# Kernel optimization log

Measured on AMD Instinct MI355X. Metric: run time of the kernel, lower is better.

The kernel has to match this reference:

```python
import jax, jax.numpy as jnp
import numpy as np

N_AGENTS = 16
OBS = 128
STATE = 256
EMBED = 32
NHID = 32
NHEADS = 4
ALPHA = 0.2  # leaky relu slope
NEG = -9.0e15


def gat_layer(h, adj, W, a):
    # h: [B,N,Fin], W: [Fin,Fout], a: [2*Fout,1]  (dropout is identity in eval mode)
    Wh = h @ W                                   # [B,N,Fout]
    f = W.shape[1]
    e = jax.nn.leaky_relu(Wh @ a[:f] + jnp.swapaxes(Wh @ a[f:], 1, 2), ALPHA)  # [B,N,N]
    att = jnp.where(adj > 0, e, NEG)
    att = jax.nn.softmax(att, axis=1)            # faithful to torch dim=1 on [B,N,N]
    return att @ Wh                              # [B,N,Fout]


def gat(x, adj, Wh_heads, a_heads, Wout, aout):
    # Wh_heads: [H,Fin,NHID], a_heads: [H,2*NHID,1]
    heads = jax.vmap(gat_layer, in_axes=(None, None, 0, 0))(x, adj, Wh_heads, a_heads)  # [H,B,N,NHID]
    heads = jax.nn.elu(heads)                    # concat=True layers apply elu
    B, N = x.shape[0], x.shape[1]
    xcat = jnp.transpose(heads, (1, 2, 0, 3)).reshape(B, N, -1)  # [B,N,H*NHID]
    out = gat_layer(xcat, adj, Wout, aout)       # concat=False: no elu inside layer
    out = jax.nn.elu(out)
    return jax.nn.log_softmax(out, axis=1)       # over agent axis, as in torch dim=1


def setup_inputs() -> dict:
    key = jax.random.key(0)
    ks = jax.random.split(key, 20)
    bs, T = 64, 128
    s = 0.05
    inp = {
        "agent_qs": jax.random.normal(ks[0], (bs, T, N_AGENTS), jnp.float32),
        "states": jax.random.normal(ks[1], (bs, T, STATE), jnp.float32),
        "obs_ls": jax.random.normal(ks[2], (bs, T, N_AGENTS, OBS), jnp.float32),
        "adj_ls": jnp.ones((bs, T, N_AGENTS, N_AGENTS), jnp.float32),
        # weight_net: Linear(STATE, N_AGENTS)
        "wn_w": jax.random.normal(ks[3], (N_AGENTS, STATE), jnp.float32) * s,
        "wn_b": jnp.zeros((N_AGENTS,), jnp.float32),
        # hyper_w_1 GAT: 4 heads (OBS->NHID), out (NHID*4 -> N_AGENTS*EMBED)
        "g1_Wh": jax.random.normal(ks[4], (NHEADS, OBS, NHID), jnp.float32) * s,
        "g1_ah": jax.random.normal(ks[5], (NHEADS, 2 * NHID, 1), jnp.float32) * s,
        "g1_Wout": jax.random.normal(ks[6], (NHID * NHEADS, N_AGENTS * EMBED), jnp.float32) * s,
        "g1_aout": jax.random.normal(ks[7], (2 * N_AGENTS * EMBED, 1), jnp.float32) * s,
        # hyper_w_final GAT: 4 heads (OBS->NHID), out (NHID*4 -> EMBED)
        "gf_Wh": jax.random.normal(ks[8], (NHEADS, OBS, NHID), jnp.float32) * s,
        "gf_ah": jax.random.normal(ks[9], (NHEADS, 2 * NHID, 1), jnp.float32) * s,
        "gf_Wout": jax.random.normal(ks[10], (NHID * NHEADS, EMBED), jnp.float32) * s,
        "gf_aout": jax.random.normal(ks[11], (2 * EMBED, 1), jnp.float32) * s,
        # hyper_b_ls: N_AGENTS Linears(STATE -> EMBED), stacked
        "hb_W": jax.random.normal(ks[12], (N_AGENTS, EMBED, STATE), jnp.float32) * s,
        "hb_b": jnp.zeros((N_AGENTS, EMBED), jnp.float32),
        # V: Linear(STATE,EMBED) -> ReLU -> Linear(EMBED,1)
        "v1_w": jax.random.normal(ks[13], (EMBED, STATE), jnp.float32) * s,
        "v1_b": jnp.zeros((EMBED,), jnp.float32),
        "v2_w": jax.random.normal(ks[14], (1, EMBED), jnp.float32) * s,
        "v2_b": jnp.zeros((1,), jnp.float32),
    }
    return inp


def reference(agent_qs, states, obs_ls, adj_ls, wn_w, wn_b,
              g1_Wh, g1_ah, g1_Wout, g1_aout,
              gf_Wh, gf_ah, gf_Wout, gf_aout,
              hb_W, hb_b, v1_w, v1_b, v2_w, v2_b):
    bs = agent_qs.shape[0]
    qs = agent_qs.reshape(-1, N_AGENTS)                 # [B,N]
    st = states.reshape(-1, STATE)                      # [B,S]
    obs = obs_ls.reshape(-1, N_AGENTS, OBS)             # [B,N,OBS]
    adj = adj_ls.reshape(-1, N_AGENTS, N_AGENTS)        # [B,N,N]
    B = qs.shape[0]

    hyper_w1 = jnp.abs(gat(obs, adj, g1_Wh, g1_ah, g1_Wout, g1_aout))   # [B,N,N*E]
    hyper_wf = jnp.abs(gat(obs, adj, gf_Wh, gf_ah, gf_Wout, gf_aout))   # [B,N,E]

    dis = jnp.abs(st @ wn_w.T + wn_b)                   # [B,N]

    w1 = hyper_w1.reshape(B, N_AGENTS, N_AGENTS, EMBED)  # [B,i,n,E]
    b_all = jnp.einsum('bs,nes->bne', st, hb_W) + hb_b   # [B,N,E]
    hidden = jax.nn.elu(jnp.einsum('bn,bine->bie', qs, w1) + b_all)  # [B,N,E]

    v = jax.nn.relu(st @ v1_w.T + v1_b) @ v2_w.T + v2_b  # [B,1]

    y = jnp.einsum('bje,bje->bj', hidden, hyper_wf)       # [B,N]
    q = jnp.einsum('bj,bj->b', y, dis) + v[:, 0]          # [B]
    return q.reshape(bs, -1, 1)
```

## Files before the change

kernel.cpp:

```cpp
#include <hip/hip_runtime.h>
#include <math.h>

#define NAG 16
#define OBSD 128
#define STATED 256
#define ALPHA 0.2f
#define NEGV -9.0e15f
#define BTOT 8192
#define SLOT_H 2432

typedef _Float16 v4h __attribute__((ext_vector_type(4)));
typedef _Float16 v8h __attribute__((ext_vector_type(8)));
typedef float v4f __attribute__((ext_vector_type(4)));

__device__ __forceinline__ float lrelu(float x){ return x > 0.f ? x : ALPHA*x; }
__device__ __forceinline__ float eluf(float x){ return x > 0.f ? x : (__expf(x)-1.f); }

#define MFMA16(A,B,C) __builtin_amdgcn_mfma_f32_16x16x16f16((A),(B),(C),0,0,0)
#define MFMA32(A,B,C) __builtin_amdgcn_mfma_f32_16x16x32_f16((A),(B),(C),0,0,0)

__global__ void prep2_kernel(const float* __restrict__ g1_Wout, const float* __restrict__ g1_aout,
                             const float* __restrict__ gf_Wout, const float* __restrict__ gf_aout,
                             float* __restrict__ wa){
  int k = threadIdx.x;
  float su = 0.f, sv = 0.f;
  for (int c = 0; c < 512; ++c){
    float w = g1_Wout[k*512 + c];
    su += w * g1_aout[c];
    sv += w * g1_aout[512 + c];
  }
  wa[k] = su; wa[128 + k] = sv;
  float fu = 0.f, fv = 0.f;
  for (int c = 0; c < 32; ++c){
    float w = gf_Wout[k*32 + c];
    fu += w * gf_aout[c];
    fv += w * gf_aout[32 + c];
  }
  wa[256 + k] = fu; wa[384 + k] = fv;
}

__global__ void pack_wh_kernel(const float* __restrict__ g1_Wh, const float* __restrict__ gf_Wh,
                               const float* __restrict__ g1_ah, const float* __restrict__ gf_ah,
                               _Float16* __restrict__ dst){
  int idx = blockIdx.x*256 + threadIdx.x;
  if (idx >= 17*2048) return;
  int j = idx & 7, lane = (idx>>3)&63, kk = (idx>>9)&3, nt = idx>>11;
  int k = kk*32 + (lane>>4)*8 + j;
  int li = lane & 15;
  float v;
  if (nt < 16){
    int g = nt>>1, c = (nt&1)*16 + li;
    v = (g<4) ? g1_Wh[(g*OBSD + k)*32 + c] : gf_Wh[((g-4)*OBSD + k)*32 + c];
  } else {
    int g = li>>1, half = li&1;
    const float* W = (g<4)? (g1_Wh + g*OBSD*32) : (gf_Wh + (g-4)*OBSD*32);
    const float* a = ((g<4)? (g1_ah + g*64) : (gf_ah + (g-4)*64)) + half*32;
    float s = 0.f;
    for (int c=0;c<32;++c) s += W[k*32+c]*a[c];
    v = s;
  }
  dst[idx] = (_Float16)v;
}

__global__ void pack_wout_kernel(const float* __restrict__ g1_Wout, const float* __restrict__ gf_Wout,
                                 _Float16* __restrict__ dst1, _Float16* __restrict__ dstf){
  int idx = blockIdx.x*256 + threadIdx.x;
  if (idx < 65536){
    int j = idx&7, lane=(idx>>3)&63, kk=(idx>>9)&3, nt=idx>>11;
    int k = kk*32 + (lane>>4)*8 + j;
    dst1[idx] = (_Float16)g1_Wout[k*512 + nt*16 + (lane&15)];
  } else {
    int i2 = idx - 65536;
    int j=i2&7, lane=(i2>>3)&63, kk=(i2>>9)&3, nt=i2>>11;
    int k = kk*32 + (lane>>4)*8 + j;
    dstf[i2] = (_Float16)gf_Wout[k*32 + nt*16 + (lane&15)];
  }
}

__global__ void pack_wst_kernel(const float* __restrict__ hb_W, const float* __restrict__ wn_w,
                                const float* __restrict__ v1_w, _Float16* __restrict__ dst){
  int idx = blockIdx.x*256 + threadIdx.x;
  if (idx >= 35*4096) return;
  int j = idx&7, lane=(idx>>3)&63, kk=(idx>>9)&7, nt=idx>>12;
  int s = kk*32 + (lane>>4)*8 + j;
  int c = nt*16 + (lane&15);
  float v;
  if (c < 512)      v = hb_W[c*STATED + s];
  else if (c < 528) v = wn_w[(c-512)*STATED + s];
  else              v = v1_w[(c-528)*STATED + s];
  dst[idx] = (_Float16)v;
}

__global__ __launch_bounds__(256) void st_kernel(
    const float* __restrict__ states,
    const _Float16* __restrict__ wstf,
    const float* __restrict__ hb_b, const float* __restrict__ wn_b,
    const float* __restrict__ v1_b, const float* __restrict__ v2_w,
    const float* __restrict__ v2_b,
    float* __restrict__ b_all, float* __restrict__ dis, float* __restrict__ vv){
  __shared__ float vh_s[16*32];
  const int t = threadIdx.x, w = t>>6, lane = t&63, lg = lane>>4, li = lane&15;
  const int b0 = blockIdx.x*16;
  const float* sp = states + (size_t)(b0+li)*STATED + lg*8;
  v8h ast[8];
  #pragma unroll
  for (int kk=0;kk<8;++kk){
    v4f f0 = *reinterpret_cast<const v4f*>(sp + kk*32);
    v4f f1 = *reinterpret_cast<const v4f*>(sp + kk*32 + 4);
    v8h h;
    #pragma unroll
    for (int jj=0;jj<4;++jj){ h[jj]=(_Float16)f0[jj]; h[4+jj]=(_Float16)f1[jj]; }
    ast[kk]=h;
  }
  for (int nt=w; nt<35; nt+=4){
    v4f d = {0.f,0.f,0.f,0.f};
    #pragma unroll
    for (int kk=0;kk<8;++kk){
      v8h bf = *reinterpret_cast<const v8h*>(wstf + (size_t)(((nt*8+kk)<<6)+lane)*8);
      d = MFMA32(ast[kk], bf, d);
    }
    int c = nt*16 + li;
    if (c < 512){
      float bias = hb_b[c];
      #pragma unroll
      for (int r=0;r<4;++r) b_all[(size_t)(b0+lg*4+r)*512 + c] = d[r]+bias;
    } else if (c < 528){
      float bias = wn_b[c-512];
      #pragma unroll
      for (int r=0;r<4;++r) dis[(b0+lg*4+r)*NAG + (c-512)] = fabsf(d[r]+bias);
    } else {
      float bias = v1_b[c-528];
      #pragma unroll
      for (int r=0;r<4;++r) vh_s[(lg*4+r)*32 + (c-528)] = fmaxf(d[r]+bias, 0.f);
    }
  }
  __syncthreads();
  if (t < 16){
    float s = v2_b[0];
    #pragma unroll
    for (int e=0;e<32;++e) s += vh_s[t*32+e]*v2_w[e];
    vv[b0+t] = s;
  }
}

__global__ __launch_bounds__(256,4) void gat_kernel(
    const float* __restrict__ agent_qs,
    const float* __restrict__ obs_ls,
    const float* __restrict__ adj_ls,
    const _Float16* __restrict__ whf,
    const _Float16* __restrict__ wo1f,
    const _Float16* __restrict__ wodf,
    const float* __restrict__ wa_g,
    const float* __restrict__ b_all_ws,
    const float* __restrict__ dis_ws,
    const float* __restrict__ vv_ws,
    float* __restrict__ out){
  __shared__ __align__(16) _Float16 arena_h[4*SLOT_H];
  __shared__ __align__(8)  _Float16 adjh[4*256];
  __shared__ float qs_s[64];

  const int t = threadIdx.x, w = t>>6, lane = t&63, lg = lane>>4, li = lane&15;
  const int bb = blockIdx.x*4;
  const int b = bb + w;
  const int eh = w&1, pb = (w>>1)*2;
  const v4f ZERO4 = {0.f,0.f,0.f,0.f};
  const v4h ONESH = {(_Float16)1.f,(_Float16)1.f,(_Float16)1.f,(_Float16)1.f};

  {
    float4 f = reinterpret_cast<const float4*>(adj_ls + (size_t)bb*256)[t];
    _Float16* ap = adjh + t*4;
    ap[0]=(_Float16)f.x; ap[1]=(_Float16)f.y; ap[2]=(_Float16)f.z; ap[3]=(_Float16)f.w;
  }
  if (t < 64) qs_s[t] = agent_qs[bb*NAG + t];

  _Float16* slot   = arena_h + w*SLOT_H;
  _Float16* att_h  = slot;
  _Float16* uv_h   = slot + 2176;
  _Float16* u2v2_h = slot;
  _Float16* att2_h = slot + 64;
  const _Float16* adjw = adjh + w*256;

  const float* ob = obs_ls + (size_t)b*(NAG*OBSD) + li*OBSD + lg*8;
  v8h aob[4];
  #pragma unroll
  for (int kk=0;kk<4;++kk){
    v4f f0 = *reinterpret_cast<const v4f*>(ob + kk*32);
    v4f f1 = *reinterpret_cast<const v4f*>(ob + kk*32 + 4);
    v8h h;
    #pragma unroll
    for (int jj=0;jj<4;++jj){ h[jj]=(_Float16)f0[jj]; h[4+jj]=(_Float16)f1[jj]; }
    aob[kk]=h;
  }
  v4h whB[16];
  #pragma unroll
  for (int nt=0;nt<16;++nt){
    v4f d = ZERO4;
    #pragma unroll
    for (int kk=0;kk<4;++kk){
      v8h bf = *reinterpret_cast<const v8h*>(whf + (size_t)(((nt*4+kk)<<6) + lane)*8);
      d = MFMA32(aob[kk], bf, d);
    }
    v4h hh;
    #pragma unroll
    for (int r=0;r<4;++r) hh[r]=(_Float16)d[r];
    whB[nt]=hh;
  }
  {
    v4f d = ZERO4;
    #pragma unroll
    for (int kk=0;kk<4;++kk){
      v8h bf = *reinterpret_cast<const v8h*>(whf + (size_t)(((64+kk)<<6) + lane)*8);
      d = MFMA32(aob[kk], bf, d);
    }
    #pragma unroll
    for (int r=0;r<4;++r)
      uv_h[(li>>1)*32 + (li&1)*16 + lg*4 + r] = (_Float16)d[r];
  }

  {
    int cc = lane*2;
    int g = cc>>4, j0 = cc&15;
    float vj0 = (float)uv_h[g*32+16+j0], vj1 = (float)uv_h[g*32+16+j0+1];
    float e0[16], e1[16];
    float s0=0.f, s1=0.f;
    #pragma unroll
    for (int i=0;i<16;++i){
      float u = (float)uv_h[g*32+i];
      union { unsigned u32; _Float16 h[2]; } aa;
      aa.u32 = *reinterpret_cast<const unsigned*>(adjw + i*16 + j0);
      float x0 = lrelu(u+vj0), x1 = lrelu(u+vj1);
      x0 = ((float)aa.h[0] > 0.f) ? x0 : NEGV;
      x1 = ((float)aa.h[1] > 0.f) ? x1 : NEGV;
      x0 = __expf(x0); x1 = __expf(x1);
      e0[i]=x0; e1[i]=x1; s0+=x0; s1+=x1;
    }
    float inv0=1.f/s0, inv1=1.f/s1;
    #pragma unroll
    for (int i=0;i<16;++i){
      union { unsigned u32; _Float16 h[2]; } pk;
      pk.h[0]=(_Float16)(e0[i]*inv0);
      pk.h[1]=(_Float16)(e1[i]*inv1);
      int blk = (j0>>2) ^ ((i>>2)&3);
      *reinterpret_cast<unsigned*>(&att_h[g*272 + i*16 + (blk<<2) + (j0&3)]) = pk.u32;
    }
  }

  v4h xcB[16];
  float p2[4][4];
  #pragma unroll
  for (int k4=0;k4<4;++k4)
    #pragma unroll
    for (int r=0;r<4;++r) p2[k4][r]=0.f;
  {
    const int ablk = (lg ^ ((li>>2)&3)) << 2;
    #pragma unroll
    for (int g=0;g<8;++g){
      v4h afr = *reinterpret_cast<const v4h*>(&att_h[g*272 + li*16 + ablk]);
      int side = g>>2;
      #pragma unroll
      for (int h2=0;h2<2;++h2){
        int nt = g*2+h2;
        v4f d = ZERO4;
        d = MFMA16(afr, whB[nt], d);
        int cl = (nt - side*8)*16 + li;
        float wu = wa_g[side*256 + cl];
        float wv = wa_g[side*256 + 128 + cl];
        v4h hh;
        #pragma unroll
        for (int r=0;r<4;++r){
          float e = eluf(d[r]);
          hh[r]=(_Float16)e;
          p2[side*2][r]   += e*wu;
          p2[side*2+1][r] += e*wv;
        }
        xcB[nt]=hh;
      }
    }
  }
  #pragma unroll
  for (int off=1; off<16; off<<=1)
    #pragma unroll
    for (int k4=0;k4<4;++k4)
      #pragma unroll
      for (int r=0;r<4;++r) p2[k4][r] += __shfl_xor(p2[k4][r], off, 64);
  if (li==0){
    #pragma unroll
    for (int k4=0;k4<4;++k4)
      #pragma unroll
      for (int r=0;r<4;++r) u2v2_h[k4*16 + lg*4 + r] = (_Float16)p2[k4][r];
  }

  if (lane < 32){
    int side = lane>>4, j = lane&15;
    float vj = (float)u2v2_h[side*32 + 16 + j];
    float ev[16]; float ss=0.f;
    #pragma unroll
    for (int i=0;i<16;++i){
      float x = lrelu((float)u2v2_h[side*32 + i] + vj);
      x = ((float)adjw[i*16+j] > 0.f) ? x : NEGV;
      x = __expf(x);
      ev[i]=x; ss+=x;
    }
    float inv=1.f/ss;
    #pragma unroll
    for (int i=0;i<16;++i) att2_h[side*288 + j*18 + i] = (_Float16)(ev[i]*inv);
  }

  v4h bat0, bat1;
  #pragma unroll
  for (int jj=0;jj<4;++jj){
    bat0[jj] = att2_h[(lg*4+jj)*18 + li];
    bat1[jj] = att2_h[288 + (lg*4+jj)*18 + li];
  }
  #pragma unroll
  for (int ct=0;ct<8;++ct){
    v4f zD = ZERO4;
    zD = MFMA16(xcB[ct], bat0, zD);
    int kk = ct>>1;
    int lp = li + 16*((ct&1)*2 + (lg>>1));
    _Float16* dst = slot + kk*512 + lp*8 + (lg&1)*4;
    union { unsigned u32; _Float16 h[2]; } q0,q1;
    q0.h[0]=(_Float16)zD[0]; q0.h[1]=(_Float16)zD[1];
    q1.h[0]=(_Float16)zD[2]; q1.h[1]=(_Float16)zD[3];
    *reinterpret_cast<unsigned*>(dst)   = q0.u32;
    *reinterpret_cast<unsigned*>(dst+2) = q1.u32;
  }
  unsigned qg0[8], qg1[8];
  #pragma unroll
  for (int ct=0;ct<8;++ct){
    v4f zD = ZERO4;
    zD = MFMA16(xcB[8+ct], bat1, zD);
    union { unsigned u32; _Float16 h[2]; } q0,q1;
    q0.h[0]=(_Float16)zD[0]; q0.h[1]=(_Float16)zD[1];
    q1.h[0]=(_Float16)zD[2]; q1.h[1]=(_Float16)zD[3];
    qg0[ct]=q0.u32; qg1[ct]=q1.u32;
  }
  __syncthreads();

  v8h az[2][4];
  #pragma unroll
  for (int bi=0;bi<2;++bi)
    #pragma unroll
    for (int kk=0;kk<4;++kk)
      az[bi][kk] = *reinterpret_cast<const v8h*>(arena_h + (pb+bi)*SLOT_H + kk*512 + lane*8);
  __syncthreads();

  #pragma unroll
  for (int ct=0;ct<8;++ct){
    int kk = ct>>1;
    int lp = li + 16*((ct&1)*2 + (lg>>1));
    _Float16* dst = slot + kk*512 + lp*8 + (lg&1)*4;
    *reinterpret_cast<unsigned*>(dst)   = qg0[ct];
    *reinterpret_cast<unsigned*>(dst+2) = qg1[ct];
  }
  v8h azf[4];
  #pragma unroll
  for (int kk=0;kk<4;++kk)
    azf[kk] = *reinterpret_cast<const v8h*>(slot + kk*512 + lane*8);
  __syncthreads();

  float hyp[2][4];
  #pragma unroll
  for (int nt2=0;nt2<2;++nt2){
    v4f d = ZERO4;
    #pragma unroll
    for (int kk=0;kk<4;++kk){
      v8h bf = *reinterpret_cast<const v8h*>(wodf + (size_t)(((nt2*4+kk)<<6)+lane)*8);
      d = MFMA32(azf[kk], bf, d);
    }
    float x[4]; v4h exh;
    #pragma unroll
    for (int r=0;r<4;++r){ x[r]=eluf(d[r]); exh[r]=(_Float16)__expf(x[r]); }
    v4f S = MFMA16(ONESH, exh, ZERO4);
    float ls = __logf(S[0]);
    #pragma unroll
    for (int r=0;r<4;++r) hyp[nt2][r] = fabsf(x[r]-ls);
  }

  {
    float pa[2][4];
    #pragma unroll
    for (int bi=0;bi<2;++bi)
      #pragma unroll
      for (int r=0;r<4;++r) pa[bi][r]=0.f;
    #pragma unroll
    for (int n=0;n<16;++n){
      int nt = n*2 + eh;
      v8h bf[4];
      #pragma unroll
      for (int kk=0;kk<4;++kk)
        bf[kk] = *reinterpret_cast<const v8h*>(wo1f + (size_t)(((nt*4+kk)<<6)+lane)*8);
      #pragma unroll
      for (int bi=0;bi<2;++bi){
        v4f d = ZERO4;
        #pragma unroll
        for (int kk=0;kk<4;++kk) d = MFMA32(az[bi][kk], bf[kk], d);
        float x[4]; v4h exh;
        #pragma unroll
        for (int r=0;r<4;++r){ x[r]=eluf(d[r]); exh[r]=(_Float16)__expf(x[r]); }
        v4f S = MFMA16(ONESH, exh, ZERO4);
        float ls = __logf(S[0]);
        float q = qs_s[(pb+bi)*16 + n];
        #pragma unroll
        for (int r=0;r<4;++r) pa[bi][r] += q*fabsf(x[r]-ls);
      }
    }
    #pragma unroll
    for (int bi=0;bi<2;++bi){
      float* pdst = reinterpret_cast<float*>(arena_h + (pb+bi)*SLOT_H) + eh*256;
      #pragma unroll
      for (int r=0;r<4;++r) pdst[(lg*4+r)*16 + li] = pa[bi][r];
    }
  }
  __syncthreads();

  {
    const float* ba = b_all_ws + (size_t)b*512;
    float ps[4] = {0.f,0.f,0.f,0.f};
    #pragma unroll
    for (int nt2=0;nt2<2;++nt2){
      const float* ph = reinterpret_cast<const float*>(slot) + nt2*256;
      #pragma unroll
      for (int r=0;r<4;++r){
        int i = lg*4+r;
        float hv = eluf(ba[i*32 + nt2*16 + li] + ph[i*16 + li]);
        ps[r] += hv * hyp[nt2][r];
      }
    }
    #pragma unroll
    for (int off=1; off<16; off<<=1)
      #pragma unroll
      for (int r=0;r<4;++r) ps[r] += __shfl_xor(ps[r], off, 64);
    float qp = 0.f;
    #pragma unroll
    for (int r=0;r<4;++r) qp += ps[r] * dis_ws[(size_t)b*NAG + lg*4 + r];
    qp += __shfl_xor(qp, 16, 64);
    qp += __shfl_xor(qp, 32, 64);
    if (lane == 0) out[b] = qp + vv_ws[b];
  }
}

extern "C" void kernel_launch(void* const* d_in, const int* in_sizes, int n_in,
                              void* d_out, int out_size, void* d_ws, size_t ws_size,
                              hipStream_t stream) {
  const float* agent_qs = (const float*)d_in[0];
  const float* states   = (const float*)d_in[1];
  const float* obs_ls   = (const float*)d_in[2];
  const float* adj_ls   = (const float*)d_in[3];
  const float* wn_w     = (const float*)d_in[4];
  const float* wn_b     = (const float*)d_in[5];
  const float* g1_Wh    = (const float*)d_in[6];
  const float* g1_ah    = (const float*)d_in[7];
  const float* g1_Wout  = (const float*)d_in[8];
  const float* g1_aout  = (const float*)d_in[9];
  const float* gf_Wh    = (const float*)d_in[10];
  const float* gf_ah    = (const float*)d_in[11];
  const float* gf_Wout  = (const float*)d_in[12];
  const float* gf_aout  = (const float*)d_in[13];
  const float* hb_W     = (const float*)d_in[14];
  const float* hb_b     = (const float*)d_in[15];
  const float* v1_w     = (const float*)d_in[16];
  const float* v1_b     = (const float*)d_in[17];
  const float* v2_w     = (const float*)d_in[18];
  const float* v2_b     = (const float*)d_in[19];

  float* ws    = (float*)d_ws;
  float* b_all = ws;
  float* dis   = b_all + (size_t)BTOT*512;
  float* vvv   = dis + (size_t)BTOT*NAG;
  float* wa    = vvv + BTOT;
  _Float16* whf  = (_Float16*)(wa + 512);
  _Float16* wo1f = whf + 34816;
  _Float16* wodf = wo1f + 65536;
  _Float16* wstf = wodf + 4096;

  prep2_kernel<<<dim3(1), dim3(128), 0, stream>>>(g1_Wout, g1_aout, gf_Wout, gf_aout, wa);
  pack_wh_kernel<<<dim3(136), dim3(256), 0, stream>>>(g1_Wh, gf_Wh, g1_ah, gf_ah, whf);
  pack_wout_kernel<<<dim3(272), dim3(256), 0, stream>>>(g1_Wout, gf_Wout, wo1f, wodf);
  pack_wst_kernel<<<dim3(560), dim3(256), 0, stream>>>(hb_W, wn_w, v1_w, wstf);
  st_kernel<<<dim3(BTOT/16), dim3(256), 0, stream>>>(states, wstf, hb_b, wn_b, v1_b, v2_w, v2_b,
                                                     b_all, dis, vvv);
  gat_kernel<<<dim3(BTOT/4), dim3(256), 0, stream>>>(agent_qs, obs_ls, adj_ls,
                                                     whf, wo1f, wodf, wa,
                                                     b_all, dis, vvv, (float*)d_out);
}
```

Baseline: 127.9 us.

## Give each wave its own batch for the hyper_w1 output projection

```diff
diff --git a/kernel.cpp b/kernel.cpp
--- a/kernel.cpp
+++ b/kernel.cpp
@@ -157,21 +157,17 @@
     float* __restrict__ out){
   __shared__ __align__(16) _Float16 arena_h[4*SLOT_H];
   __shared__ __align__(8)  _Float16 adjh[4*256];
-  __shared__ float qs_s[64];
 
   const int t = threadIdx.x, w = t>>6, lane = t&63, lg = lane>>4, li = lane&15;
-  const int bb = blockIdx.x*4;
-  const int b = bb + w;
-  const int eh = w&1, pb = (w>>1)*2;
+  const int b = blockIdx.x*4 + w;
   const v4f ZERO4 = {0.f,0.f,0.f,0.f};
   const v4h ONESH = {(_Float16)1.f,(_Float16)1.f,(_Float16)1.f,(_Float16)1.f};
 
   {
-    float4 f = reinterpret_cast<const float4*>(adj_ls + (size_t)bb*256)[t];
+    float4 f = reinterpret_cast<const float4*>(adj_ls + (size_t)(blockIdx.x*4)*256)[t];
     _Float16* ap = adjh + t*4;
     ap[0]=(_Float16)f.x; ap[1]=(_Float16)f.y; ap[2]=(_Float16)f.z; ap[3]=(_Float16)f.w;
   }
-  if (t < 64) qs_s[t] = agent_qs[bb*NAG + t];
 
   _Float16* slot   = arena_h + w*SLOT_H;
   _Float16* att_h  = slot;
@@ -325,39 +321,27 @@
     *reinterpret_cast<unsigned*>(dst)   = q0.u32;
     *reinterpret_cast<unsigned*>(dst+2) = q1.u32;
   }
-  unsigned qg0[8], qg1[8];
+  v8h az[4];
+  #pragma unroll
+  for (int kk=0;kk<4;++kk)
+    az[kk] = *reinterpret_cast<const v8h*>(slot + kk*512 + lane*8);
   #pragma unroll
   for (int ct=0;ct<8;++ct){
     v4f zD = ZERO4;
     zD = MFMA16(xcB[8+ct], bat1, zD);
+    int kk = ct>>1;
+    int lp = li + 16*((ct&1)*2 + (lg>>1));
+    _Float16* dst = slot + kk*512 + lp*8 + (lg&1)*4;
     union { unsigned u32; _Float16 h[2]; } q0,q1;
     q0.h[0]=(_Float16)zD[0]; q0.h[1]=(_Float16)zD[1];
     q1.h[0]=(_Float16)zD[2]; q1.h[1]=(_Float16)zD[3];
-    qg0[ct]=q0.u32; qg1[ct]=q1.u32;
-  }
-  __syncthreads();
-
-  v8h az[2][4];
-  #pragma unroll
-  for (int bi=0;bi<2;++bi)
-    #pragma unroll
-    for (int kk=0;kk<4;++kk)
-      az[bi][kk] = *reinterpret_cast<const v8h*>(arena_h + (pb+bi)*SLOT_H + kk*512 + lane*8);
-  __syncthreads();
-
-  #pragma unroll
-  for (int ct=0;ct<8;++ct){
-    int kk = ct>>1;
-    int lp = li + 16*((ct&1)*2 + (lg>>1));
-    _Float16* dst = slot + kk*512 + lp*8 + (lg&1)*4;
-    *reinterpret_cast<unsigned*>(dst)   = qg0[ct];
-    *reinterpret_cast<unsigned*>(dst+2) = qg1[ct];
+    *reinterpret_cast<unsigned*>(dst)   = q0.u32;
+    *reinterpret_cast<unsigned*>(dst+2) = q1.u32;
   }
   v8h azf[4];
   #pragma unroll
   for (int kk=0;kk<4;++kk)
     azf[kk] = *reinterpret_cast<const v8h*>(slot + kk*512 + lane*8);
-  __syncthreads();
 
   float hyp[2][4];
   #pragma unroll
@@ -377,53 +361,42 @@
     for (int r=0;r<4;++r) hyp[nt2][r] = fabsf(x[r]-ls);
   }
 
-  {
-    float pa[2][4];
-    #pragma unroll
-    for (int bi=0;bi<2;++bi)
-      #pragma unroll
-      for (int r=0;r<4;++r) pa[bi][r]=0.f;
-    #pragma unroll
-    for (int n=0;n<16;++n){
-      int nt = n*2 + eh;
-      v8h bf[4];
-      #pragma unroll
-      for (int kk=0;kk<4;++kk)
-        bf[kk] = *reinterpret_cast<const v8h*>(wo1f + (size_t)(((nt*4+kk)<<6)+lane)*8);
-      #pragma unroll
-      for (int bi=0;bi<2;++bi){
-        v4f d = ZERO4;
-        #pragma unroll
-        for (int kk=0;kk<4;++kk) d = MFMA32(az[bi][kk], bf[kk], d);
-        float x[4]; v4h exh;
-        #pragma unroll
-        for (int r=0;r<4;++r){ x[r]=eluf(d[r]); exh[r]=(_Float16)__expf(x[r]); }
-        v4f S = MFMA16(ONESH, exh, ZERO4);
-        float ls = __logf(S[0]);
-        float q = qs_s[(pb+bi)*16 + n];
-        #pragma unroll
-        for (int r=0;r<4;++r) pa[bi][r] += q*fabsf(x[r]-ls);
+  float pa[2][4];
+  #pragma unroll
+  for (int e2=0;e2<2;++e2)
+    #pragma unroll
+    for (int r=0;r<4;++r) pa[e2][r]=0.f;
+  #pragma unroll 4
+  for (int n=0;n<16;++n){
+    float q = agent_qs[b*NAG + n];
+    #pragma unroll
+    for (int e2=0;e2<2;++e2){
+      int nt = n*2 + e2;
+      v4f d = ZERO4;
+      #pragma unroll
+      for (int kk=0;kk<4;++kk){
+        v8h bf = *reinterpret_cast<const v8h*>(wo1f + (size_t)(((nt*4+kk)<<6)+lane)*8);
+        d = MFMA32(az[kk], bf, d);
       }
-    }
-    #pragma unroll
-    for (int bi=0;bi<2;++bi){
-      float* pdst = reinterpret_cast<float*>(arena_h + (pb+bi)*SLOT_H) + eh*256;
-      #pragma unroll
-      for (int r=0;r<4;++r) pdst[(lg*4+r)*16 + li] = pa[bi][r];
-    }
-  }
-  __syncthreads();
+      float x[4]; v4h exh;
+      #pragma unroll
+      for (int r=0;r<4;++r){ x[r]=eluf(d[r]); exh[r]=(_Float16)__expf(x[r]); }
+      v4f S = MFMA16(ONESH, exh, ZERO4);
+      float ls = __logf(S[0]);
+      #pragma unroll
+      for (int r=0;r<4;++r) pa[e2][r] += q*fabsf(x[r]-ls);
+    }
+  }
 
   {
     const float* ba = b_all_ws + (size_t)b*512;
     float ps[4] = {0.f,0.f,0.f,0.f};
     #pragma unroll
     for (int nt2=0;nt2<2;++nt2){
-      const float* ph = reinterpret_cast<const float*>(slot) + nt2*256;
       #pragma unroll
       for (int r=0;r<4;++r){
         int i = lg*4+r;
-        float hv = eluf(ba[i*32 + nt2*16 + li] + ph[i*16 + li]);
+        float hv = eluf(ba[i*32 + nt2*16 + li] + pa[nt2][r]);
         ps[r] += hv * hyp[nt2][r];
       }
     }
```

Measured after the change: 132.7 us. 3.8% more time.
